# Performance work log

Measured on AMD Instinct MI355X. Metric: run time of the kernel, lower is better.

## Reference

```python
import jax, jax.numpy as jnp
import numpy as np

CHANNELS = 512
COND_DIM = 768
NUM_HEADS = 8
NUM_GROUPS = 32
EPS = 1e-5


def setup_inputs() -> dict:
    key = jax.random.key(0)
    ks = jax.random.split(key, 8)
    B, H, W, C, S = 8, 64, 64, CHANNELS, 256
    x = jax.random.normal(ks[0], (B, H, W, C), dtype=jnp.float32)
    cond_tokens = jax.random.normal(ks[1], (B, S, COND_DIM), dtype=jnp.float32)
    gn_scale = jnp.ones((C,), dtype=jnp.float32)
    gn_bias = jnp.zeros((C,), dtype=jnp.float32)
    Wq = jax.random.normal(ks[2], (C, CHANNELS), dtype=jnp.float32) * 0.02
    Wk = jax.random.normal(ks[3], (COND_DIM, CHANNELS), dtype=jnp.float32) * 0.02
    Wv = jax.random.normal(ks[4], (COND_DIM, CHANNELS), dtype=jnp.float32) * 0.02
    Wo = jax.random.normal(ks[5], (CHANNELS, CHANNELS), dtype=jnp.float32) * 0.02
    bo = jnp.zeros((CHANNELS,), dtype=jnp.float32)
    return {"x": x, "cond_tokens": cond_tokens, "gn_scale": gn_scale,
            "gn_bias": gn_bias, "Wq": Wq, "Wk": Wk, "Wv": Wv, "Wo": Wo, "bo": bo}


def group_norm(x, scale, bias):
    # x: (B,H,W,C); normalize over H,W and channels within each of NUM_GROUPS groups
    b, h, w, c = x.shape
    xg = x.reshape(b, h, w, NUM_GROUPS, c // NUM_GROUPS)
    mean = jnp.mean(xg, axis=(1, 2, 4), keepdims=True)
    var = jnp.var(xg, axis=(1, 2, 4), keepdims=True)
    xn = (xg - mean) * jax.lax.rsqrt(var + EPS)
    return xn.reshape(b, h, w, c) * scale + bias


def reference(x, cond_tokens, gn_scale, gn_bias, Wq, Wk, Wv, Wo, bo):
    b, h, w, c = x.shape
    head_dim = CHANNELS // NUM_HEADS
    x_seq = group_norm(x, gn_scale, gn_bias).reshape(b, h * w, c)
    # projections
    q = (x_seq @ Wq).reshape(b, -1, NUM_HEADS, head_dim).transpose(0, 2, 1, 3)
    k = (cond_tokens @ Wk).reshape(b, -1, NUM_HEADS, head_dim).transpose(0, 2, 1, 3)
    v = (cond_tokens @ Wv).reshape(b, -1, NUM_HEADS, head_dim).transpose(0, 2, 1, 3)
    scores = jnp.einsum('bhqd,bhkd->bhqk', q, k) / np.sqrt(head_dim).astype(np.float32)
    attn = jax.nn.softmax(scores, axis=-1)
    out = jnp.einsum('bhqk,bhkd->bhqd', attn, v)
    out = out.transpose(0, 2, 1, 3).reshape(b, h * w, CHANNELS)
    out = out @ Wo + bo
    return x + out.reshape(b, h, w, c)
```

## Files before the change

kernel.cpp:

```cpp
#include <hip/hip_runtime.h>
#include <hip/hip_bf16.h>

typedef unsigned short u16;
typedef unsigned int u32;
typedef __attribute__((ext_vector_type(8))) __bf16 bf16x8;
typedef __attribute__((ext_vector_type(4))) float f32x4;
typedef __attribute__((ext_vector_type(16))) float f32x16;
typedef __attribute__((ext_vector_type(4))) u32 u32x4;

#define SCL 0.18033688011112042f

#define DEVFN static __device__ __forceinline__

DEVFN float bf2f(u16 v) { union { u32 u; float f; } x; x.u = (u32)v << 16; return x.f; }
DEVFN u16 f2bf(float f) {
    union { float f; u32 u; } x; x.f = f;
    u32 r = x.u + 0x7fff + ((x.u >> 16) & 1);
    return (u16)(r >> 16);
}

union BF2 { struct { __bf16 lo, hi; } s; u32 w; };
DEVFN u32 pk2(float a, float b) { BF2 t; t.s.lo = (__bf16)a; t.s.hi = (__bf16)b; return t.w; }

DEVFN void gload_lds16(const u16* g, u16* l) {
    __builtin_amdgcn_global_load_lds((const __attribute__((address_space(1))) u32*)g,
                                     (__attribute__((address_space(3))) u32*)l, 16, 0, 0);
}

template<int OUTMODE, bool BIAS, bool RES, bool PERB, bool RESBF>
__global__ __launch_bounds__(256)
void gemm_bt(const u16* __restrict__ A, const u16* __restrict__ B,
             const u16* __restrict__ B2,
             void* __restrict__ Cv, void* __restrict__ Cv2,
             const float* __restrict__ bias, const void* __restrict__ res,
             int K, int lda, int ldb, int ldc, float scale)
{
    __shared__ u16 smem[24576];
    const int tid = threadIdx.x;
    const int lane = tid & 63, wave = tid >> 6;
    const int wr = wave >> 1, wc = wave & 1;
    const u16* Bsel = (OUTMODE == 3 && blockIdx.z) ? B2 : B;
    if constexpr (PERB) Bsel += (long)(blockIdx.x >> 5) * 262144;
    const u16* Bb = Bsel + (long)blockIdx.y * 128 * ldb;
    const u16* Ab = A + (long)blockIdx.x * 128 * lda;
    const int sr = (tid >> 6) * 16 + (tid & 15);
    const int sc2 = ((tid >> 4) & 3) * 8;

    f32x4 acc[4][4];
#pragma unroll
    for (int i = 0; i < 4; ++i)
#pragma unroll
        for (int j = 0; j < 4; ++j) acc[i][j] = (f32x4){0.f, 0.f, 0.f, 0.f};

    const int nt = K >> 5;
    auto stage = [&](int t, u16* buf) {
#pragma unroll
        for (int p = 0; p < 2; ++p)
            gload_lds16(Ab + (long)(p * 64 + sr) * lda + t * 32 + sc2,
                        buf + (p * 256 + tid) * 8);
#pragma unroll
        for (int p = 0; p < 2; ++p)
            gload_lds16(Bb + (long)(p * 64 + sr) * ldb + t * 32 + sc2,
                        buf + 4096 + (p * 256 + tid) * 8);
    };

    stage(0, smem);
    stage(1, smem + 8192);
    int cur = 0;
    for (int t = 0; t < nt; ++t) {
        if (t + 1 < nt) asm volatile("s_waitcnt vmcnt(4)" ::: "memory");
        else            asm volatile("s_waitcnt vmcnt(0)" ::: "memory");
        __builtin_amdgcn_s_barrier();
        asm volatile("" ::: "memory");
        u16* cA = smem + cur * 8192;
        u16* cB = cA + 4096;
        int nx2 = cur + 2; if (nx2 >= 3) nx2 -= 3;
        if (t + 2 < nt) stage(t + 2, smem + nx2 * 8192);
        bf16x8 av[4], bv[4];
#pragma unroll
        for (int i = 0; i < 4; ++i) av[i] = *(const bf16x8*)(cA + (wr * 4 + i) * 512 + lane * 8);
#pragma unroll
        for (int j = 0; j < 4; ++j) bv[j] = *(const bf16x8*)(cB + (wc * 4 + j) * 512 + lane * 8);
        __builtin_amdgcn_s_setprio(1);
#pragma unroll
        for (int i = 0; i < 4; ++i)
#pragma unroll
            for (int j = 0; j < 4; ++j)
                acc[i][j] = __builtin_amdgcn_mfma_f32_16x16x32_bf16(av[i], bv[j], acc[i][j], 0, 0, 0);
        __builtin_amdgcn_s_setprio(0);
        cur = (cur + 1 == 3) ? 0 : cur + 1;
    }

    const int m0 = blockIdx.x * 128 + wr * 64 + (lane >> 4) * 4;
    const int n0 = blockIdx.y * 128 + wc * 64 + (lane & 15);
    if constexpr (OUTMODE == 0) {
        u16* Cb = (u16*)Cv;
        const float* bp = bias;
        if constexpr (PERB && BIAS) bp += (blockIdx.x >> 5) * 512;
#pragma unroll
        for (int i = 0; i < 4; ++i)
#pragma unroll
            for (int j = 0; j < 4; ++j) {
                int n = n0 + j * 16;
                float bv_ = BIAS ? bp[n] : 0.f;
#pragma unroll
                for (int r = 0; r < 4; ++r) {
                    int m = m0 + i * 16 + r;
                    Cb[(long)m * ldc + n] = f2bf(acc[i][j][r] * scale + bv_);
                }
            }
    } else if constexpr (OUTMODE == 1) {
        float* cl = (float*)smem;
        float* Co = (float*)Cv;
#pragma unroll
        for (int i = 0; i < 4; ++i) {
            __syncthreads();
#pragma unroll
            for (int j = 0; j < 4; ++j)
#pragma unroll
                for (int r = 0; r < 4; ++r) {
                    int rl = wr * 16 + (lane >> 4) * 4 + r;
                    int col = wc * 64 + j * 16 + (lane & 15);
                    cl[rl * 132 + col] = acc[i][j][r];
                }
            __syncthreads();
            int rl = tid >> 3;
            int c0 = (tid & 7) * 16;
            long m = (long)blockIdx.x * 128 + i * 16 + (rl & 15) + (rl >> 4) * 64;
            long n = (long)blockIdx.y * 128 + c0;
#pragma unroll
            for (int q = 0; q < 4; ++q) {
                float4 v = *(float4*)(cl + rl * 132 + c0 + q * 4);
                float4 o;
                o.x = v.x * scale; o.y = v.y * scale;
                o.z = v.z * scale; o.w = v.w * scale;
                if constexpr (BIAS) {
                    float4 b4 = *(const float4*)(bias + n + q * 4);
                    o.x += b4.x; o.y += b4.y; o.z += b4.z; o.w += b4.w;
                }
                if constexpr (RES) {
                    if constexpr (RESBF) {
                        ushort4 r4 = *(const ushort4*)((const u16*)res + m * ldc + n + q * 4);
                        o.x += bf2f(r4.x); o.y += bf2f(r4.y);
                        o.z += bf2f(r4.z); o.w += bf2f(r4.w);
                    } else {
                        float4 r4 = *(const float4*)((const float*)res + m * ldc + n + q * 4);
                        o.x += r4.x; o.y += r4.y; o.z += r4.z; o.w += r4.w;
                    }
                }
                *(float4*)(Co + m * ldc + n + q * 4) = o;
            }
        }
    } else {
        if (blockIdx.z == 0) {
            u16* Cb = (u16*)Cv;
#pragma unroll
            for (int i = 0; i < 4; ++i)
#pragma unroll
                for (int j = 0; j < 4; ++j) {
                    int n = n0 + j * 16;
#pragma unroll
                    for (int r = 0; r < 4; ++r) {
                        int m = m0 + i * 16 + r;
                        Cb[(long)m * ldc + n] = f2bf(acc[i][j][r] * scale);
                    }
                }
        } else {
#pragma unroll
            for (int i = 0; i < 4; ++i) {
                int m = m0 + i * 16;
                int b = m >> 8, s = m & 255;
#pragma unroll
                for (int j = 0; j < 4; ++j) {
                    int n = n0 + j * 16;
                    int h = n >> 6, d = n & 63;
                    ushort4 pk;
                    pk.x = f2bf(acc[i][j][0]); pk.y = f2bf(acc[i][j][1]);
                    pk.z = f2bf(acc[i][j][2]); pk.w = f2bf(acc[i][j][3]);
                    *(ushort4*)((u16*)Cv2 + (((long)(b * 8 + h) * 64 + d) * 256 + s)) = pk;
                }
            }
        }
    }
}

union U8 { u32 w[4]; bf16x8 v; };

__global__ __launch_bounds__(512, 4)
void attn_fused(const u16* __restrict__ Q, const u16* __restrict__ K,
                const u16* __restrict__ Vt, u16* __restrict__ O)
{
    __shared__ u16 lds[40960];
    const int tid = threadIdx.x, lane = tid & 63, wave = tid >> 6;
    const int bh = blockIdx.y, b = bh >> 3, h = bh & 7;
    const int l31 = lane & 31, lh = lane >> 5;
    const long q0 = (long)b * 4096 + blockIdx.x * 256 + wave * 32;
    const bool hiHalf = (lh != 0);

    {
        const u16* Kb_ = K + (long)b * 256 * 512 + h * 64;
        const u16* Vb_ = Vt + (long)bh * 16384;
#pragma unroll
        for (int it = 0; it < 4; ++it) {
            int f = it * 8 + wave;
            int st = f >> 2, kc = f & 3;
            gload_lds16(Kb_ + (long)(st * 32 + l31) * 512 + kc * 16 + lh * 8,
                        lds + f * 512 + lane * 8);
            int dt = f >> 4, ks = f & 15;
            gload_lds16(Vb_ + (long)(dt * 32 + l31) * 256 + ks * 16 + lh * 8,
                        lds + 16384 + f * 512 + lane * 8);
        }
    }
    bf16x8 qf[4];
    {
        const u16* Qp = Q + (q0 + l31) * 512 + h * 64 + lh * 8;
#pragma unroll
        for (int kc = 0; kc < 4; ++kc) qf[kc] = *(const bf16x8*)(Qp + kc * 16);
    }
    asm volatile("s_waitcnt vmcnt(0)" ::: "memory");
    __syncthreads();

    f32x16 oacc[2];
#pragma unroll
    for (int dt = 0; dt < 2; ++dt)
#pragma unroll
        for (int r = 0; r < 16; ++r) oacc[dt][r] = 0.f;
    float m_run = -3e38f, sum_run = 0.f;

#pragma unroll
    for (int st = 0; st < 8; ++st) {
        f32x16 sc;
#pragma unroll
        for (int r = 0; r < 16; ++r) sc[r] = 0.f;
        __builtin_amdgcn_s_setprio(1);
#pragma unroll
        for (int kc = 0; kc < 4; ++kc) {
            bf16x8 af = *(const bf16x8*)(lds + (st * 4 + kc) * 512 + lane * 8);
            sc = __builtin_amdgcn_mfma_f32_32x32x16_bf16(af, qf[kc], sc, 0, 0, 0);
        }
        __builtin_amdgcn_s_setprio(0);
        float tm = sc[0];
#pragma unroll
        for (int r = 1; r < 16; ++r) tm = fmaxf(tm, sc[r]);
        tm = fmaxf(tm, __shfl_xor(tm, 32));
        if (!__all(tm <= m_run + 8.f)) {
            float mnew = fmaxf(m_run, tm);
            float fac = exp2f(m_run - mnew);
            m_run = mnew;
            sum_run *= fac;
#pragma unroll
            for (int dt = 0; dt < 2; ++dt)
#pragma unroll
                for (int r = 0; r < 16; ++r) oacc[dt][r] *= fac;
        }
#pragma unroll
        for (int r = 0; r < 16; ++r) {
            float e = exp2f(sc[r] - m_run);
            sc[r] = e; sum_run += e;
        }
        u32 c[8], x[8];
#pragma unroll
        for (int i = 0; i < 8; ++i) c[i] = pk2(sc[2 * i], sc[2 * i + 1]);
#pragma unroll
        for (int i = 0; i < 8; ++i) x[i] = (u32)__shfl_xor((int)c[i], 32);
        U8 p0, p1;
        p0.w[0] = hiHalf ? x[2] : c[0];  p0.w[1] = hiHalf ? x[3] : c[1];
        p0.w[2] = hiHalf ? c[2] : x[0];  p0.w[3] = hiHalf ? c[3] : x[1];
        p1.w[0] = hiHalf ? x[6] : c[4];  p1.w[1] = hiHalf ? x[7] : c[5];
        p1.w[2] = hiHalf ? c[6] : x[4];  p1.w[3] = hiHalf ? c[7] : x[5];
        __builtin_amdgcn_s_setprio(1);
#pragma unroll
        for (int dt = 0; dt < 2; ++dt) {
            bf16x8 v0 = *(const bf16x8*)(lds + 16384 + (dt * 16 + st * 2) * 512 + lane * 8);
            bf16x8 v1 = *(const bf16x8*)(lds + 16384 + (dt * 16 + st * 2 + 1) * 512 + lane * 8);
            oacc[dt] = __builtin_amdgcn_mfma_f32_32x32x16_bf16(v0, p0.v, oacc[dt], 0, 0, 0);
            oacc[dt] = __builtin_amdgcn_mfma_f32_32x32x16_bf16(v1, p1.v, oacc[dt], 0, 0, 0);
        }
        __builtin_amdgcn_s_setprio(0);
    }

    sum_run += __shfl_xor(sum_run, 32);
    float inv = 1.f / sum_run;

    u16* ow = lds + 32768 + (wave & 3) * 2048;
    const int shift = wave >> 2;
#pragma unroll
    for (int s_ = 0; s_ < 2; ++s_) {
        if (s_ == 1) __syncthreads();
        if (shift == s_) {
            const int q = l31;
#pragma unroll
            for (int dt = 0; dt < 2; ++dt)
#pragma unroll
                for (int rq = 0; rq < 4; ++rq) {
                    int d = dt * 32 + rq * 8 + 4 * lh;
                    u32 w0 = pk2(oacc[dt][rq * 4 + 0] * inv, oacc[dt][rq * 4 + 1] * inv);
                    u32 w1 = pk2(oacc[dt][rq * 4 + 2] * inv, oacc[dt][rq * 4 + 3] * inv);
                    int byte = q * 128 + ((d * 2) ^ ((q & 7) << 4));
                    *(u32*)((char*)ow + byte) = w0;
                    *(u32*)((char*)ow + byte + 4) = w1;
                }
#pragma unroll
            for (int i = 0; i < 4; ++i) {
                int qq = (lane >> 3) + i * 8;
                int byte = qq * 128 + (((lane & 7) * 16) ^ ((qq & 7) << 4));
                bf16x8 val = *(const bf16x8*)((char*)ow + byte);
                *(bf16x8*)(O + (q0 + qq) * 512 + h * 64 + (lane & 7) * 8) = val;
            }
        }
    }
}

__global__ __launch_bounds__(256)
void gn_part(const float* __restrict__ x, float* __restrict__ part,
             u16* __restrict__ xb)
{
    const int b = blockIdx.x, ch = blockIdx.y;
    const long base = ((long)b * 4096 + ch * 64) * 512;
    const float* bx = x + base;
    u16* bo = xb + base;
    const int t = threadIdx.x;
    const int c4 = t & 127, r0 = t >> 7;
    float sum = 0.f, sq = 0.f;
    for (int rr = r0; rr < 64; rr += 2) {
        float4 v = *(const float4*)(bx + (long)rr * 512 + c4 * 4);
        sum += v.x + v.y + v.z + v.w;
        sq  += v.x * v.x + v.y * v.y + v.z * v.z + v.w * v.w;
        uint2 w;
        w.x = pk2(v.x, v.y); w.y = pk2(v.z, v.w);
        *(uint2*)(bo + (long)rr * 512 + c4 * 4) = w;
    }
    __shared__ float s0[128], s1[128];
    if (t >= 128) { s0[c4] = sum; s1[c4] = sq; }
    __syncthreads();
    if (t < 128) {
        sum += s0[c4]; sq += s1[c4];
        sum += __shfl_down(sum, 2); sum += __shfl_down(sum, 1);
        sq  += __shfl_down(sq, 2);  sq  += __shfl_down(sq, 1);
        if ((t & 3) == 0) {
            int g = t >> 2;
            float* pp = part + (long)(b * 64 + ch) * 64;
            pp[g] = sum; pp[32 + g] = sq;
        }
    }
}

__global__ __launch_bounds__(256)
void gn_coef(const float* __restrict__ part, const float* __restrict__ gscale,
             const float* __restrict__ gbias, float* __restrict__ coefA,
             float* __restrict__ coefD)
{
    const int t = threadIdx.x;
    const int b = t >> 5, g = t & 31;
    float S = 0.f, Q = 0.f;
    for (int ch = 0; ch < 64; ++ch) {
        const float* pp = part + (long)(b * 64 + ch) * 64;
        S += pp[g]; Q += pp[32 + g];
    }
    float mean = S * (1.f / 65536.f);
    float var = Q * (1.f / 65536.f) - mean * mean;
    float rstd = rsqrtf(var + 1e-5f);
#pragma unroll
    for (int cc = 0; cc < 16; ++cc) {
        int c = g * 16 + cc;
        float a = gscale[c] * rstd;
        coefA[b * 512 + c] = a;
        coefD[b * 512 + c] = gbias[c] - mean * a;
    }
}

__global__ __launch_bounds__(256)
void scale_wq(const float* __restrict__ Wq, const float* __restrict__ cfA,
              u16* __restrict__ WqS)
{
    __shared__ u16 t[32][33];
    const int b = blockIdx.z;
    const int r0 = blockIdx.y * 32, c0 = blockIdx.x * 32;
    int tx = threadIdx.x & 31, ty = threadIdx.x >> 5;
    for (int i = ty; i < 32; i += 8)
        t[i][tx] = f2bf(Wq[(long)(r0 + i) * 512 + c0 + tx] * cfA[b * 512 + r0 + i] * SCL);
    __syncthreads();
    for (int i = ty; i < 32; i += 8)
        WqS[(long)b * 262144 + (long)(c0 + i) * 512 + r0 + tx] = t[tx][i];
}

__global__ __launch_bounds__(256)
void dq_bias(const float* __restrict__ Wq, const float* __restrict__ cfD,
             float* __restrict__ dq)
{
    const int b = blockIdx.x, nc = blockIdx.y;
    const int t = threadIdx.x;
    const int n = nc * 64 + (t & 63);
    const int cq = t >> 6;
    float a = 0.f;
    for (int c = cq * 128; c < cq * 128 + 128; ++c)
        a += cfD[b * 512 + c] * Wq[(long)c * 512 + n];
    __shared__ float red[256];
    red[t] = a;
    __syncthreads();
    if (t < 64) {
        float s = red[t] + red[64 + t] + red[128 + t] + red[192 + t];
        dq[b * 512 + nc * 64 + t] = s * SCL;
    }
}

__global__ __launch_bounds__(256)
void conv_bf16(const float* __restrict__ in, u16* __restrict__ out)
{
    long e = ((long)blockIdx.x * 256 + threadIdx.x) * 8;
    float4 v0 = *(const float4*)(in + e);
    float4 v1 = *(const float4*)(in + e + 4);
    float f[8] = { v0.x, v0.y, v0.z, v0.w, v1.x, v1.y, v1.z, v1.w };
    u32x4 o;
#pragma unroll
    for (int q = 0; q < 4; ++q)
        o[q] = (u32)f2bf(f[q * 2]) | ((u32)f2bf(f[q * 2 + 1]) << 16);
    *(u32x4*)(out + e) = o;
}

__global__ __launch_bounds__(256)
void transpose_all(const float* __restrict__ Wk, const float* __restrict__ Wv,
                   const float* __restrict__ Wo,
                   u16* __restrict__ WkT, u16* __restrict__ WvT,
                   u16* __restrict__ WoT)
{
    __shared__ u16 t[32][33];
    const int z = blockIdx.z;
    const float* in = (z == 0) ? Wk : (z == 1) ? Wv : Wo;
    u16* out = (z == 0) ? WkT : (z == 1) ? WvT : WoT;
    const int R = (z < 2) ? 768 : 512, C = 512;
    const int r0 = blockIdx.y * 32, c0 = blockIdx.x * 32;
    if (r0 >= R) return;
    int tx = threadIdx.x & 31, ty = threadIdx.x >> 5;
    for (int i = ty; i < 32; i += 8) t[i][tx] = f2bf(in[(long)(r0 + i) * C + c0 + tx]);
    __syncthreads();
    for (int i = ty; i < 32; i += 8) out[(long)(c0 + i) * R + r0 + tx] = t[tx][i];
}

extern "C" void kernel_launch(void* const* d_in, const int* in_sizes, int n_in,
                              void* d_out, int out_size, void* d_ws, size_t ws_size,
                              hipStream_t stream)
{
    const float* x    = (const float*)d_in[0];
    const float* cond = (const float*)d_in[1];
    const float* gsc  = (const float*)d_in[2];
    const float* gbi  = (const float*)d_in[3];
    const float* Wq   = (const float*)d_in[4];
    const float* Wk   = (const float*)d_in[5];
    const float* Wv   = (const float*)d_in[6];
    const float* Wo   = (const float*)d_in[7];
    const float* bo   = (const float*)d_in[8];

    char* ws = (char*)d_ws;
    size_t off = 0;
    auto alloc = [&](size_t bytes) -> void* {
        void* p = ws + off; off += (bytes + 255) & ~(size_t)255; return p;
    };
    u16* WkT    = (u16*)alloc(512 * 768 * 2);
    u16* WvT    = (u16*)alloc(512 * 768 * 2);
    u16* WoT    = (u16*)alloc(512 * 512 * 2);
    u16* WqS    = (u16*)alloc(8l * 512 * 512 * 2);
    float* cfA  = (float*)alloc(8 * 512 * 4);
    float* cfD  = (float*)alloc(8 * 512 * 4);
    float* dq   = (float*)alloc(8 * 512 * 4);
    float* part = (float*)alloc(8 * 64 * 64 * 4);
    u16* condb  = (u16*)alloc(2048l * 768 * 2);
    u16* xb     = (u16*)alloc(33554432);
    u16* Ob     = (u16*)alloc(33554432);
    u16* Qb     = (u16*)alloc(33554432);
    u16* Kb     = (u16*)alloc(2048l * 512 * 2);
    u16* Vt     = (u16*)alloc(2097152);

    transpose_all<<<dim3(16, 24, 3), 256, 0, stream>>>(Wk, Wv, Wo, WkT, WvT, WoT);
    conv_bf16<<<768, 256, 0, stream>>>(cond, condb);

    gn_part<<<dim3(8, 64), 256, 0, stream>>>(x, part, xb);
    gn_coef<<<1, 256, 0, stream>>>(part, gsc, gbi, cfA, cfD);
    scale_wq<<<dim3(16, 16, 8), 256, 0, stream>>>(Wq, cfA, WqS);
    dq_bias<<<dim3(8, 8), 256, 0, stream>>>(Wq, cfD, dq);

    gemm_bt<3, false, false, false, false><<<dim3(16, 4, 2), 256, 0, stream>>>(
        condb, WkT, WvT, Kb, Vt, nullptr, nullptr, 768, 768, 768, 512, 1.f);

    gemm_bt<0, true, false, true, false><<<dim3(256, 4), 256, 0, stream>>>(
        xb, WqS, nullptr, Qb, nullptr, dq, nullptr, 512, 512, 512, 512, 1.f);

    attn_fused<<<dim3(16, 64), 512, 0, stream>>>(Qb, Kb, Vt, Ob);

    gemm_bt<1, true, true, false, true><<<dim3(256, 4), 256, 0, stream>>>(
        Ob, WoT, nullptr, d_out, nullptr, bo, xb, 512, 512, 512, 512, 1.f);
}
```

Measured before the change: 218.7 us.

## Use double-buffered GEMM pipeline and swizzle block order for XCD locality

The GEMM drops from a triple-buffered LDS pipeline with two tiles in flight to a double-buffered one that waits for all loads and does a full barrier each iteration. This cuts LDS use from 48KB to 32KB per block, which may raise occupancy. It also adds a block-index swizzle for the Q and output projections that remaps block IDs so consecutive M tiles sharing an A row block land on the same XCD group, aiming at better L2 reuse. The cost is less overlap between loads and compute, since the loads for the next tile are now only one step ahead.

Measured after the change: 226.7 us. 3.7% more time.

```diff
diff --git a/kernel.cpp b/kernel.cpp
--- a/kernel.cpp
+++ b/kernel.cpp
@@ -27,7 +27,7 @@
                                      (__attribute__((address_space(3))) u32*)l, 16, 0, 0);
 }
 
-template<int OUTMODE, bool BIAS, bool RES, bool PERB, bool RESBF>
+template<int OUTMODE, bool BIAS, bool RES, bool PERB, bool RESBF, bool SWZ>
 __global__ __launch_bounds__(256)
 void gemm_bt(const u16* __restrict__ A, const u16* __restrict__ B,
              const u16* __restrict__ B2,
@@ -35,14 +35,20 @@
              const float* __restrict__ bias, const void* __restrict__ res,
              int K, int lda, int ldb, int ldc, float scale)
 {
-    __shared__ u16 smem[24576];
+    __shared__ u16 smem[16384];
     const int tid = threadIdx.x;
     const int lane = tid & 63, wave = tid >> 6;
     const int wr = wave >> 1, wc = wave & 1;
+    int bx, by;
+    if constexpr (SWZ) {
+        int id = blockIdx.y * gridDim.x + blockIdx.x;
+        int idx = (id & 7) * ((gridDim.x * 4) >> 3) + (id >> 3);
+        bx = idx >> 2; by = idx & 3;
+    } else { bx = blockIdx.x; by = blockIdx.y; }
     const u16* Bsel = (OUTMODE == 3 && blockIdx.z) ? B2 : B;
-    if constexpr (PERB) Bsel += (long)(blockIdx.x >> 5) * 262144;
-    const u16* Bb = Bsel + (long)blockIdx.y * 128 * ldb;
-    const u16* Ab = A + (long)blockIdx.x * 128 * lda;
+    if constexpr (PERB) Bsel += (long)(bx >> 5) * 262144;
+    const u16* Bb = Bsel + (long)by * 128 * ldb;
+    const u16* Ab = A + (long)bx * 128 * lda;
     const int sr = (tid >> 6) * 16 + (tid & 15);
     const int sc2 = ((tid >> 4) & 3) * 8;
 
@@ -65,17 +71,14 @@
     };
 
     stage(0, smem);
-    stage(1, smem + 8192);
     int cur = 0;
     for (int t = 0; t < nt; ++t) {
-        if (t + 1 < nt) asm volatile("s_waitcnt vmcnt(4)" ::: "memory");
-        else            asm volatile("s_waitcnt vmcnt(0)" ::: "memory");
-        __builtin_amdgcn_s_barrier();
-        asm volatile("" ::: "memory");
+        asm volatile("s_waitcnt vmcnt(0)" ::: "memory");
+        __syncthreads();
+        const int nxt = cur ^ 1;
         u16* cA = smem + cur * 8192;
         u16* cB = cA + 4096;
-        int nx2 = cur + 2; if (nx2 >= 3) nx2 -= 3;
-        if (t + 2 < nt) stage(t + 2, smem + nx2 * 8192);
+        if (t + 1 < nt) stage(t + 1, smem + nxt * 8192);
         bf16x8 av[4], bv[4];
 #pragma unroll
         for (int i = 0; i < 4; ++i) av[i] = *(const bf16x8*)(cA + (wr * 4 + i) * 512 + lane * 8);
@@ -88,15 +91,15 @@
             for (int j = 0; j < 4; ++j)
                 acc[i][j] = __builtin_amdgcn_mfma_f32_16x16x32_bf16(av[i], bv[j], acc[i][j], 0, 0, 0);
         __builtin_amdgcn_s_setprio(0);
-        cur = (cur + 1 == 3) ? 0 : cur + 1;
-    }
-
-    const int m0 = blockIdx.x * 128 + wr * 64 + (lane >> 4) * 4;
-    const int n0 = blockIdx.y * 128 + wc * 64 + (lane & 15);
+        cur = nxt;
+    }
+
+    const int m0 = bx * 128 + wr * 64 + (lane >> 4) * 4;
+    const int n0 = by * 128 + wc * 64 + (lane & 15);
     if constexpr (OUTMODE == 0) {
         u16* Cb = (u16*)Cv;
         const float* bp = bias;
-        if constexpr (PERB && BIAS) bp += (blockIdx.x >> 5) * 512;
+        if constexpr (PERB && BIAS) bp += (bx >> 5) * 512;
 #pragma unroll
         for (int i = 0; i < 4; ++i)
 #pragma unroll
@@ -126,8 +129,8 @@
             __syncthreads();
             int rl = tid >> 3;
             int c0 = (tid & 7) * 16;
-            long m = (long)blockIdx.x * 128 + i * 16 + (rl & 15) + (rl >> 4) * 64;
-            long n = (long)blockIdx.y * 128 + c0;
+            long m = (long)bx * 128 + i * 16 + (rl & 15) + (rl >> 4) * 64;
+            long n = (long)by * 128 + c0;
 #pragma unroll
             for (int q = 0; q < 4; ++q) {
                 float4 v = *(float4*)(cl + rl * 132 + c0 + q * 4);
@@ -479,14 +482,14 @@
     scale_wq<<<dim3(16, 16, 8), 256, 0, stream>>>(Wq, cfA, WqS);
     dq_bias<<<dim3(8, 8), 256, 0, stream>>>(Wq, cfD, dq);
 
-    gemm_bt<3, false, false, false, false><<<dim3(16, 4, 2), 256, 0, stream>>>(
+    gemm_bt<3, false, false, false, false, false><<<dim3(16, 4, 2), 256, 0, stream>>>(
         condb, WkT, WvT, Kb, Vt, nullptr, nullptr, 768, 768, 768, 512, 1.f);
 
-    gemm_bt<0, true, false, true, false><<<dim3(256, 4), 256, 0, stream>>>(
+    gemm_bt<0, true, false, true, false, true><<<dim3(256, 4), 256, 0, stream>>>(
         xb, WqS, nullptr, Qb, nullptr, dq, nullptr, 512, 512, 512, 512, 1.f);
 
     attn_fused<<<dim3(16, 64), 512, 0, stream>>>(Qb, Kb, Vt, Ob);
 
-    gemm_bt<1, true, true, false, true><<<dim3(256, 4), 256, 0, stream>>>(
+    gemm_bt<1, true, true, false, true, true><<<dim3(256, 4), 256, 0, stream>>>(
         Ob, WoT, nullptr, d_out, nullptr, bo, xb, 512, 512, 512, 512, 1.f);
 }
```
